# Kernel tuning notes

Hardware: AMD Instinct MI355X
Metric: run time of the kernel (lower is better)

Reference implementation:

```python
import jax, jax.numpy as jnp
import numpy as np

B = 4096       # batch
D = 256        # num_features
H = 512        # proposal_hidden_units
K = 10         # mixture_components
C = 64         # context_units
L = 4          # proposal_residual_blocks
S = 10         # num_importance_samples (call default)
HEAD = 3 * K + C
LOG2PI = float(np.log(2.0 * np.pi))


def setup_inputs() -> dict:
    key = jax.random.key(0)
    ks = jax.random.split(key, 10)
    x = jax.random.normal(ks[0], (B, D), jnp.float32)
    observed_mask = (jax.random.uniform(ks[1], (B, D)) < 0.5).astype(jnp.float32)
    s_in = 1.0 / np.sqrt(2 * D)
    s_h = 1.0 / np.sqrt(H)
    W_in = (jax.random.normal(ks[2], (2 * D, H), jnp.float32) * s_in)
    b_in = jnp.zeros((H,), jnp.float32)
    W1 = jax.random.normal(ks[3], (L, H, H), jnp.float32) * s_h
    b1 = jnp.zeros((L, H), jnp.float32)
    W2 = jax.random.normal(ks[4], (L, H, H), jnp.float32) * s_h
    b2 = jnp.zeros((L, H), jnp.float32)
    W_fin = jax.random.normal(ks[5], (H, D * HEAD), jnp.float32) * s_h
    b_fin = jnp.zeros((D * HEAD,), jnp.float32)
    return {
        "x": x, "observed_mask": observed_mask,
        "W_in": W_in, "b_in": b_in,
        "W1": W1, "b1": b1, "W2": W2, "b2": b2,
        "W_fin": W_fin, "b_fin": b_fin,
        "num_importance_samples": S,
    }


def _proposal_params(x_o, observed_mask, W_in, b_in, W1, b1, W2, b2, W_fin, b_fin):
    # Residual MLP proposal network on [x_o, observed_mask].
    h = jnp.concatenate([x_o, observed_mask], axis=-1) @ W_in + b_in  # [B, H]
    for l in range(L):
        r = jax.nn.relu(h) @ W1[l] + b1[l]
        r = jax.nn.relu(r) @ W2[l] + b2[l]
        h = h + r
    out = (h @ W_fin + b_fin).reshape(h.shape[0], D, HEAD)  # [B, D, 3K+C]
    logits = out[..., :K]
    means = out[..., K:2 * K]
    scales = jax.nn.softplus(out[..., 2 * K:3 * K]) + 1e-3
    return logits, means, scales


def reference(x, observed_mask, W_in, b_in, W1, b1, W2, b2, W_fin, b_fin,
              num_importance_samples):
    query = 1.0 - observed_mask
    x_o = x * observed_mask
    x_u = x * query

    logits, means, scales = _proposal_params(
        x_o, observed_mask, W_in, b_in, W1, b1, W2, b2, W_fin, b_fin)

    # Per-feature mixture-of-Gaussians log-likelihood of x_u, masked by query.
    log_w = jax.nn.log_softmax(logits, axis=-1)               # [B, D, K]
    z = (x_u[..., None] - means) / scales
    comp_ll = -0.5 * z * z - jnp.log(scales) - 0.5 * LOG2PI   # [B, D, K]
    proposal_ll = jax.scipy.special.logsumexp(log_w + comp_ll, axis=-1) * query

    # Samples (stop_gradient in the original).
    skey = jax.random.key(1234)
    kc, kn = jax.random.split(skey)
    comp = jax.random.categorical(kc, logits, axis=-1,
                                  shape=(num_importance_samples,) + logits.shape[:2])  # [S, B, D]
    mu = jnp.take_along_axis(means[None], comp[..., None], axis=-1)[..., 0]    # [S, B, D]
    sg = jnp.take_along_axis(scales[None], comp[..., None], axis=-1)[..., 0]   # [S, B, D]
    eps = jax.random.normal(kn, comp.shape, jnp.float32)
    samples = mu + sg * eps                                   # [S, B, D]
    samples = jnp.transpose(samples, (1, 0, 2))               # [B, S, D]
    samples = jax.lax.stop_gradient(samples) * query[:, None, :]
    # call() multiplies by query twice (before and after selected_features block)
    proposal_samples = samples * query[:, None, :]

    proposal_mean = jnp.sum(jax.nn.softmax(logits, axis=-1) * means, axis=-1) * query
    proposal_mean = proposal_mean * query  # second masking, as in call()

    return proposal_ll, proposal_samples, proposal_mean
```

## Files before the change

### kernel.cpp

```cpp
#include <hip/hip_runtime.h>
#include <cstdint>

#define B 4096
#define D 256
#define H 512
#define K 10
#define NL 4
#define S 10
#define NOUT 30
#define HEADW 94
#define ND (B*D)
#define NFIN 7680
#define NLOG 2560
#define NMS  5120

typedef __bf16 bf16x8 __attribute__((ext_vector_type(8)));
typedef float  f32x16 __attribute__((ext_vector_type(16)));

__host__ __device__ inline void threefry2x32(uint32_t k0, uint32_t k1,
                                             uint32_t x0, uint32_t x1,
                                             uint32_t& o0, uint32_t& o1) {
  uint32_t ks2 = k0 ^ k1 ^ 0x1BD11BDAu;
#define TF_ROT(x, r) (((x) << (r)) | ((x) >> (32 - (r))))
#define TF_RND(r) { x0 += x1; x1 = TF_ROT(x1, r); x1 ^= x0; }
  x0 += k0; x1 += k1;
  TF_RND(13) TF_RND(15) TF_RND(26) TF_RND(6)
  x0 += k1; x1 += ks2 + 1u;
  TF_RND(17) TF_RND(29) TF_RND(16) TF_RND(24)
  x0 += ks2; x1 += k0 + 2u;
  TF_RND(13) TF_RND(15) TF_RND(26) TF_RND(6)
  x0 += k0; x1 += k1 + 3u;
  TF_RND(17) TF_RND(29) TF_RND(16) TF_RND(24)
  x0 += k1; x1 += ks2 + 4u;
  TF_RND(13) TF_RND(15) TF_RND(26) TF_RND(6)
  x0 += ks2; x1 += k0 + 5u;
  o0 = x0; o1 = x1;
#undef TF_RND
#undef TF_ROT
}

__device__ __forceinline__ uint32_t rb32(uint32_t k0, uint32_t k1, uint32_t idx) {
  uint32_t a, b;
  threefry2x32(k0, k1, 0u, idx, a, b);
  return a ^ b;
}

__device__ __forceinline__ float u01_from_bits(uint32_t bits) {
  return __uint_as_float((bits >> 9) | 0x3f800000u) - 1.0f;
}

__device__ __forceinline__ float erfinv_f32(float x) {
  float w = -log1pf(-x * x);
  float p;
  if (w < 5.0f) {
    w = w - 2.5f;
    p = 2.81022636e-08f;
    p = fmaf(p, w, 3.43273939e-07f);
    p = fmaf(p, w, -3.5233877e-06f);
    p = fmaf(p, w, -4.39150654e-06f);
    p = fmaf(p, w, 0.00021858087f);
    p = fmaf(p, w, -0.00125372503f);
    p = fmaf(p, w, -0.00417768164f);
    p = fmaf(p, w, 0.246640727f);
    p = fmaf(p, w, 1.50140941f);
  } else {
    w = sqrtf(w) - 3.0f;
    p = -0.000200214257f;
    p = fmaf(p, w, 0.000100950558f);
    p = fmaf(p, w, 0.00134934322f);
    p = fmaf(p, w, -0.00367342844f);
    p = fmaf(p, w, 0.00573950773f);
    p = fmaf(p, w, -0.0076224613f);
    p = fmaf(p, w, 0.00943887047f);
    p = fmaf(p, w, 1.00167406f);
    p = fmaf(p, w, 2.83297682f);
  }
  return p * x;
}

__device__ __forceinline__ unsigned short bf16_rne(float x) {
  uint32_t u = __float_as_uint(x);
  uint32_t r = u + 0x7fffu + ((u >> 16) & 1u);
  return (unsigned short)(r >> 16);
}

__device__ __forceinline__ void split2(float x, short& hi, short& lo) {
  unsigned short hb = bf16_rne(x);
  float hf = __uint_as_float((uint32_t)hb << 16);
  hi = (short)hb;
  lo = (short)bf16_rne(x - hf);
}

__device__ __forceinline__ void gload16(const void* g, void* l) {
  __builtin_amdgcn_global_load_lds(
      (const __attribute__((address_space(1))) void*)g,
      (__attribute__((address_space(3))) void*)l, 16, 0, 0);
}

template <int ROWS>
__device__ __forceinline__ void stage_region(const short* __restrict__ g,
                                             short* l, int wid, int lane) {
#pragma unroll
  for (int c = wid; c < ROWS / 16; c += 4) {
    const short* gp = g + (size_t)(c * 16 + (lane >> 2)) * 512 + (lane & 3) * 8;
    gload16(gp, l + c * 512);
  }
}

__global__ __launch_bounds__(256) void prep_kernel(const float* __restrict__ x,
                                                   const float* __restrict__ mask,
                                                   float* __restrict__ xcat) {
  int i = blockIdx.x * 256 + threadIdx.x;
  if (i >= B * 2 * D) return;
  int b = i >> 9, c = i & 511;
  float v = (c < D) ? x[b * D + c] * mask[b * D + c] : mask[b * D + (c - D)];
  xcat[i] = v;
}

__global__ __launch_bounds__(256) void wgatherL(const float* __restrict__ Wf,
                                                float* __restrict__ wsgL) {
  int c = blockIdx.x * 256 + threadIdx.x;
  int k = blockIdx.y;
  int dd = c / K, j = c - dd * K;
  wsgL[(size_t)k * NLOG + c] = Wf[(size_t)k * (D * HEADW) + dd * HEADW + j];
}

__global__ __launch_bounds__(256) void wsplit_ms(const float* __restrict__ Wf,
                                                 short* __restrict__ whi,
                                                 short* __restrict__ wlo) {
  __shared__ float tile[32][33];
  int n0 = blockIdx.x * 32, k0 = blockIdx.y * 32;
  int tx = threadIdx.x & 31, ty = threadIdx.x >> 5;
#pragma unroll
  for (int r = 0; r < 4; ++r) {
    int k = k0 + ty + r * 8;
    int n = n0 + tx;
    int dd = n / 20, j = n - dd * 20;
    tile[ty + r * 8][tx] = Wf[(size_t)k * (D * HEADW) + dd * HEADW + 10 + j];
  }
  __syncthreads();
#pragma unroll
  for (int r = 0; r < 4; ++r) {
    int n = n0 + ty + r * 8;
    int k = k0 + tx;
    float v = tile[tx][ty + r * 8];
    short hb, lb;
    split2(v, hb, lb);
    whi[(size_t)n * 512 + k] = hb;
    wlo[(size_t)n * 512 + k] = lb;
  }
}

template <int RELU, int RES>
__global__ __launch_bounds__(256) void gemm_trunk(const float* __restrict__ A,
                                                  const float* __restrict__ W,
                                                  const float* __restrict__ bias,
                                                  const float* res, float* C) {
  __shared__ float As[64 * 68];
  __shared__ float Ws[64 * 64];
  const int tid = threadIdx.x;
  const int lane = tid & 63, wid = tid >> 6;
  const int tx = tid & 15, ty = tid >> 4;
  const int bm = blockIdx.y * 64, bn = blockIdx.x * 64;
  const int ls = tid & 15, lm = tid >> 4;

  float acc[4][4] = {};

  for (int k0 = 0; k0 < H; k0 += 64) {
#pragma unroll
    for (int c = wid; c < 16; c += 4) {
      gload16(W + (size_t)(k0 + c * 4 + (lane >> 4)) * H + bn + (lane & 15) * 4,
              Ws + c * 256 + lane * 4);
    }
#pragma unroll
    for (int r = 0; r < 4; ++r) {
      int m = lm + 16 * r;
      float4 f = *(const float4*)(A + (size_t)(bm + m) * H + k0 + 4 * ls);
      if (RELU) {
        f.x = fmaxf(f.x, 0.0f); f.y = fmaxf(f.y, 0.0f);
        f.z = fmaxf(f.z, 0.0f); f.w = fmaxf(f.w, 0.0f);
      }
      As[(4 * ls + 0) * 68 + m] = f.x;
      As[(4 * ls + 1) * 68 + m] = f.y;
      As[(4 * ls + 2) * 68 + m] = f.z;
      As[(4 * ls + 3) * 68 + m] = f.w;
    }
    __syncthreads();
#pragma unroll
    for (int kk = 0; kk < 64; ++kk) {
      float4 a4 = *(const float4*)(As + kk * 68 + ty * 4);
      float4 b4 = *(const float4*)(Ws + kk * 64 + tx * 4);
      float a[4] = {a4.x, a4.y, a4.z, a4.w};
      float b[4] = {b4.x, b4.y, b4.z, b4.w};
#pragma unroll
      for (int i = 0; i < 4; ++i)
#pragma unroll
        for (int j = 0; j < 4; ++j) acc[i][j] = fmaf(a[i], b[j], acc[i][j]);
    }
    __syncthreads();
  }
#pragma unroll
  for (int i = 0; i < 4; ++i) {
    int row = bm + ty * 4 + i;
#pragma unroll
    for (int j = 0; j < 4; ++j) {
      int col = bn + tx * 4 + j;
      float v = acc[i][j] + bias[col];
      if (RES) v = res[(size_t)row * H + col] + v;
      C[(size_t)row * H + col] = v;
    }
  }
}

__global__ __launch_bounds__(256) void gemm_head(const float* __restrict__ A,
                                                 const float* __restrict__ Wg,
                                                 const short* __restrict__ Bh,
                                                 const short* __restrict__ Bl,
                                                 const float* __restrict__ bf,
                                                 float* __restrict__ headout) {
  __shared__ __align__(16) float smem[8448];
  const int tid = threadIdx.x;
  const int lane = tid & 63, wid = tid >> 6;
  const int bm = blockIdx.y * 128;

  if (blockIdx.x < 20) {
    float* As = smem;
    float* Ws = smem + 4352;
    const int tx = tid & 15, ty = tid >> 4;
    const int bn = blockIdx.x * 128;
    const int ls = tid & 7, lm = tid >> 3;

    float acc[8][8] = {};

    for (int k0 = 0; k0 < H; k0 += 32) {
#pragma unroll
      for (int c = wid; c < 16; c += 4) {
        gload16(Wg + (size_t)(k0 + c * 2 + (lane >> 5)) * NLOG + bn + (lane & 31) * 4,
                Ws + c * 256 + lane * 4);
      }
#pragma unroll
      for (int r = 0; r < 4; ++r) {
        int m = lm + 32 * r;
        float4 f = *(const float4*)(A + (size_t)(bm + m) * H + k0 + 4 * ls);
        As[(4 * ls + 0) * 136 + m] = f.x;
        As[(4 * ls + 1) * 136 + m] = f.y;
        As[(4 * ls + 2) * 136 + m] = f.z;
        As[(4 * ls + 3) * 136 + m] = f.w;
      }
      __syncthreads();
#pragma unroll
      for (int kk = 0; kk < 32; ++kk) {
        float a[8], b[8];
        *(float4*)(a + 0) = *(const float4*)(As + kk * 136 + ty * 8);
        *(float4*)(a + 4) = *(const float4*)(As + kk * 136 + ty * 8 + 4);
        *(float4*)(b + 0) = *(const float4*)(Ws + kk * 128 + tx * 8);
        *(float4*)(b + 4) = *(const float4*)(Ws + kk * 128 + tx * 8 + 4);
#pragma unroll
        for (int i = 0; i < 8; ++i)
#pragma unroll
          for (int j = 0; j < 8; ++j) acc[i][j] = fmaf(a[i], b[j], acc[i][j]);
      }
      __syncthreads();
    }
#pragma unroll
    for (int i = 0; i < 8; ++i) {
      int row = bm + ty * 8 + i;
#pragma unroll
      for (int j = 0; j < 8; ++j) {
        int c = bn + tx * 8 + j;
        int dd = c / K, jj = c - dd * K;
        float v = acc[i][j] + bf[dd * HEADW + jj];
        headout[(size_t)row * NFIN + dd * NOUT + jj] = v;
      }
    }
  } else {
    short* lds = (short*)smem;
    const int wm = wid >> 1, wn = wid & 1;
    const int bn = (blockIdx.x - 20) * 128;
    const int ls = tid & 7, lm = tid >> 3;

    short* ldsAh = lds;
    short* ldsAl = lds + 4096;
    short* ldsBh = lds + 8192;
    short* ldsBl = lds + 12288;

    const short* gBh = Bh + (size_t)bn * 512;
    const short* gBl = Bl + (size_t)bn * 512;

    f32x16 acc[2][2];
#pragma unroll
    for (int mt = 0; mt < 2; ++mt)
#pragma unroll
      for (int nt = 0; nt < 2; ++nt)
#pragma unroll
        for (int i = 0; i < 16; ++i) acc[mt][nt][i] = 0.0f;

    for (int k0 = 0; k0 < 512; k0 += 32) {
      stage_region<128>(gBh + k0, ldsBh, wid, lane);
      stage_region<128>(gBl + k0, ldsBl, wid, lane);
#pragma unroll
      for (int r = 0; r < 4; ++r) {
        int m = lm + 32 * r;
        float4 f = *(const float4*)(A + (size_t)(bm + m) * H + k0 + 4 * ls);
        short4 h4, l4;
        split2(f.x, h4.x, l4.x); split2(f.y, h4.y, l4.y);
        split2(f.z, h4.z, l4.z); split2(f.w, h4.w, l4.w);
        *(short4*)(ldsAh + m * 32 + 4 * ls) = h4;
        *(short4*)(ldsAl + m * 32 + 4 * ls) = l4;
      }
      __syncthreads();
#pragma unroll
      for (int sub = 0; sub < 2; ++sub) {
        bf16x8 ah[2], al[2], bh[2], bl[2];
#pragma unroll
        for (int mt = 0; mt < 2; ++mt) {
          int r = wm * 64 + mt * 32 + (lane & 31);
          int off = r * 32 + sub * 16 + (lane >> 5) * 8;
          ah[mt] = *(const bf16x8*)(ldsAh + off);
          al[mt] = *(const bf16x8*)(ldsAl + off);
        }
#pragma unroll
        for (int nt = 0; nt < 2; ++nt) {
          int r = wn * 64 + nt * 32 + (lane & 31);
          int off = r * 32 + sub * 16 + (lane >> 5) * 8;
          bh[nt] = *(const bf16x8*)(ldsBh + off);
          bl[nt] = *(const bf16x8*)(ldsBl + off);
        }
#pragma unroll
        for (int mt = 0; mt < 2; ++mt)
#pragma unroll
          for (int nt = 0; nt < 2; ++nt) {
            acc[mt][nt] = __builtin_amdgcn_mfma_f32_32x32x16_bf16(ah[mt], bh[nt], acc[mt][nt], 0, 0, 0);
            acc[mt][nt] = __builtin_amdgcn_mfma_f32_32x32x16_bf16(ah[mt], bl[nt], acc[mt][nt], 0, 0, 0);
            acc[mt][nt] = __builtin_amdgcn_mfma_f32_32x32x16_bf16(al[mt], bh[nt], acc[mt][nt], 0, 0, 0);
          }
      }
      __syncthreads();
    }

#pragma unroll
    for (int mt = 0; mt < 2; ++mt)
#pragma unroll
      for (int nt = 0; nt < 2; ++nt) {
        int col = bn + wn * 64 + nt * 32 + (lane & 31);
        int rbase = bm + wm * 64 + mt * 32 + 4 * (lane >> 5);
        int dd = col / 20, j = col - dd * 20;
#pragma unroll
        for (int reg = 0; reg < 16; ++reg) {
          int row = rbase + (reg & 3) + 8 * (reg >> 2);
          float v = acc[mt][nt][reg] + bf[dd * HEADW + 10 + j];
          if (j >= 10) v = (fmaxf(v, 0.0f) + log1pf(expf(-fabsf(v)))) + 0.001f;
          headout[(size_t)row * NFIN + dd * NOUT + 10 + j] = v;
        }
      }
  }
}

__global__ __launch_bounds__(256) void init_counter(int* counter) {
  if (threadIdx.x == 0 && blockIdx.x == 0) *counter = 0;
}

__global__ __launch_bounds__(256) void compact_zero(const float* __restrict__ mask,
                                                    float* __restrict__ out_ll,
                                                    float* __restrict__ out_s,
                                                    float* __restrict__ out_mean,
                                                    int* __restrict__ list,
                                                    int* __restrict__ counter) {
  int idx = blockIdx.x * 256 + threadIdx.x;
  if (idx >= ND) return;
  if (mask[idx] != 0.0f) {
    int b = idx >> 8, d = idx & (D - 1);
    out_ll[idx] = 0.0f;
    out_mean[idx] = 0.0f;
#pragma unroll
    for (int s = 0; s < S; ++s) out_s[((size_t)b * S + s) * D + d] = 0.0f;
  } else {
    int pos = atomicAdd(counter, 1);
    list[pos] = idx;
  }
}

__global__ __launch_bounds__(256) void fused_tail(const float* __restrict__ head,
                                                  const float* __restrict__ x,
                                                  const float* __restrict__ mask,
                                                  const int* __restrict__ list,
                                                  const int* __restrict__ counter,
                                                  float* __restrict__ out_ll,
                                                  float* __restrict__ out_s,
                                                  float* __restrict__ out_mean,
                                                  uint32_t kc0, uint32_t kc1,
                                                  uint32_t kn0, uint32_t kn1) {
  int i = blockIdx.x * 256 + threadIdx.x;
  if (i >= *counter) return;
  int idx = list[i];
  int b = idx >> 8, d = idx & (D - 1);
  const float* hp = head + (size_t)idx * NOUT;
  float lg[K], mn[K], sc[K];
#pragma unroll
  for (int k = 0; k < K; ++k) { lg[k] = hp[k]; mn[k] = hp[K + k]; sc[k] = hp[2 * K + k]; }
  float q = 1.0f - mask[idx];
  float xu = x[idx] * q;
  float m = lg[0];
#pragma unroll
  for (int k = 1; k < K; ++k) m = fmaxf(m, lg[k]);
  float e[K];
  float sum = 0.0f;
#pragma unroll
  for (int k = 0; k < K; ++k) { e[k] = expf(lg[k] - m); sum += e[k]; }
  float lse = logf(sum);
  float a[K];
  float amax = -3.402823466e38f;
#pragma unroll
  for (int k = 0; k < K; ++k) {
    float z = (xu - mn[k]) / sc[k];
    float cll = -0.5f * z * z - logf(sc[k]) - 0.9189385332046727f;
    float lw = (lg[k] - m) - lse;
    a[k] = lw + cll;
    amax = fmaxf(amax, a[k]);
  }
  float s2 = 0.0f;
#pragma unroll
  for (int k = 0; k < K; ++k) s2 += expf(a[k] - amax);
  out_ll[idx] = (logf(s2) + amax) * q;
  float pm = 0.0f;
#pragma unroll
  for (int k = 0; k < K; ++k) pm += (e[k] / sum) * mn[k];
  out_mean[idx] = pm * q;
  float inv_e[K];
#pragma unroll
  for (int k = 0; k < K; ++k) inv_e[k] = 1.0f / e[k];
  for (int s = 0; s < S; ++s) {
    uint32_t t32 = (uint32_t)s * (uint32_t)ND + (uint32_t)idx;
    uint32_t base = t32 * (uint32_t)K;
    int best = 0;
    float rbest = 3.402823466e38f;
#pragma unroll
    for (int k = 0; k < K; ++k) {
      uint32_t bits = rb32(kc0, kc1, base + (uint32_t)k);
      float u = u01_from_bits(bits);
      float wv = -__log2f(u);
      float r = wv * inv_e[k];
      if (r < rbest) { rbest = r; best = k; }
    }
    uint32_t ebits = rb32(kn0, kn1, t32);
    float f = u01_from_bits(ebits);
    float r2 = f * 2.0f + (-0.99999994f);
    r2 = fmaxf(r2, -0.99999994f);
    float eps = 1.4142135623730951f * erfinv_f32(r2);
    out_s[((size_t)b * S + s) * D + d] = (mn[best] + sc[best] * eps) * q;
  }
}

extern "C" void kernel_launch(void* const* d_in, const int* in_sizes, int n_in,
                              void* d_out, int out_size, void* d_ws, size_t ws_size,
                              hipStream_t stream) {
  const float* x    = (const float*)d_in[0];
  const float* mask = (const float*)d_in[1];
  const float* W_in = (const float*)d_in[2];
  const float* b_in = (const float*)d_in[3];
  const float* W1   = (const float*)d_in[4];
  const float* b1   = (const float*)d_in[5];
  const float* W2   = (const float*)d_in[6];
  const float* b2   = (const float*)d_in[7];
  const float* Wf   = (const float*)d_in[8];
  const float* bf   = (const float*)d_in[9];

  char* w = (char*)d_ws;
  float* head   = (float*)w;
  float* xcat   = head;
  float* t      = head;
  float* h      = (float*)(w + 125829120);
  float* wsgL   = (float*)(w + 134217728);
  int*   list   = (int*)(w + 134217728);
  short* wms_h  = (short*)(w + 139460608);
  short* wms_l  = (short*)(w + 144703488);
  int*   counter = (int*)(w + 149946368);

  float* out_ll   = (float*)d_out;
  float* out_s    = out_ll + (size_t)ND;
  float* out_mean = out_s + (size_t)ND * S;

  wgatherL<<<dim3(NLOG / 256, 512), 256, 0, stream>>>(Wf, wsgL);
  wsplit_ms<<<dim3(NMS / 32, 512 / 32), 256, 0, stream>>>(Wf, wms_h, wms_l);

  prep_kernel<<<(B * 2 * D) / 256, 256, 0, stream>>>(x, mask, xcat);

  dim3 gtr(H / 64, B / 64);
  gemm_trunk<0, 0><<<gtr, 256, 0, stream>>>(xcat, W_in, b_in, nullptr, h);
  for (int l = 0; l < NL; ++l) {
    gemm_trunk<1, 0><<<gtr, 256, 0, stream>>>(h, W1 + (size_t)l * H * H,
                                              b1 + (size_t)l * H, nullptr, t);
    gemm_trunk<1, 1><<<gtr, 256, 0, stream>>>(t, W2 + (size_t)l * H * H,
                                              b2 + (size_t)l * H, h, h);
  }

  gemm_head<<<dim3(60, B / 128), 256, 0, stream>>>(h, wsgL, wms_h, wms_l, bf, head);

  init_counter<<<1, 256, 0, stream>>>(counter);
  compact_zero<<<ND / 256, 256, 0, stream>>>(mask, out_ll, out_s, out_mean,
                                             list, counter);

  uint32_t kc0, kc1, kn0, kn1;
  threefry2x32(0u, 1234u, 0u, 0u, kc0, kc1);
  threefry2x32(0u, 1234u, 0u, 1u, kn0, kn1);
  fused_tail<<<ND / 256, 256, 0, stream>>>(head, x, mask, list, counter,
                                           out_ll, out_s, out_mean,
                                           kc0, kc1, kn0, kn1);
}
```

Baseline: 1.213 ms.

## Pre-tile head weights for contiguous LDS staging and skip observed-feature stores

The split bf16 head weights are now stored pre-tiled in (n-block, k-chunk, sub, half, row, 8) order, so each k-step copies contiguous 512-short chunks into LDS. The A operand in LDS gets a matching layout, which changes the MFMA fragment reads and should reduce bank conflicts. The fp32 logits path reads B with a split tx*4 / 64+tx*4 pattern to avoid LDS conflicts. Both epilogues read the mask and skip writing head outputs for observed features, since the tail only uses query positions. This adds a mask load for every output element.

```diff
diff --git a/kernel.cpp b/kernel.cpp
--- a/kernel.cpp
+++ b/kernel.cpp
@@ -97,16 +97,6 @@
       (__attribute__((address_space(3))) void*)l, 16, 0, 0);
 }
 
-template <int ROWS>
-__device__ __forceinline__ void stage_region(const short* __restrict__ g,
-                                             short* l, int wid, int lane) {
-#pragma unroll
-  for (int c = wid; c < ROWS / 16; c += 4) {
-    const short* gp = g + (size_t)(c * 16 + (lane >> 2)) * 512 + (lane & 3) * 8;
-    gload16(gp, l + c * 512);
-  }
-}
-
 __global__ __launch_bounds__(256) void prep_kernel(const float* __restrict__ x,
                                                    const float* __restrict__ mask,
                                                    float* __restrict__ xcat) {
@@ -146,8 +136,11 @@
     float v = tile[tx][ty + r * 8];
     short hb, lb;
     split2(v, hb, lb);
-    whi[(size_t)n * 512 + k] = hb;
-    wlo[(size_t)n * 512 + k] = lb;
+    int nb = n >> 7, nl = n & 127;
+    int kc = k >> 5, sub = (k >> 4) & 1, kh = (k >> 3) & 1, e = k & 7;
+    size_t idx = ((((size_t)(nb * 16 + kc) * 4 + sub * 2 + kh) * 128 + nl) * 8) + e;
+    whi[idx] = hb;
+    wlo[idx] = lb;
   }
 }
 
@@ -217,6 +210,7 @@
                                                  const short* __restrict__ Bh,
                                                  const short* __restrict__ Bl,
                                                  const float* __restrict__ bf,
+                                                 const float* __restrict__ msk,
                                                  float* __restrict__ headout) {
   __shared__ __align__(16) float smem[8448];
   const int tid = threadIdx.x;
@@ -253,8 +247,8 @@
         float a[8], b[8];
         *(float4*)(a + 0) = *(const float4*)(As + kk * 136 + ty * 8);
         *(float4*)(a + 4) = *(const float4*)(As + kk * 136 + ty * 8 + 4);
-        *(float4*)(b + 0) = *(const float4*)(Ws + kk * 128 + tx * 8);
-        *(float4*)(b + 4) = *(const float4*)(Ws + kk * 128 + tx * 8 + 4);
+        *(float4*)(b + 0) = *(const float4*)(Ws + kk * 128 + tx * 4);
+        *(float4*)(b + 4) = *(const float4*)(Ws + kk * 128 + 64 + tx * 4);
 #pragma unroll
         for (int i = 0; i < 8; ++i)
 #pragma unroll
@@ -267,8 +261,9 @@
       int row = bm + ty * 8 + i;
 #pragma unroll
       for (int j = 0; j < 8; ++j) {
-        int c = bn + tx * 8 + j;
+        int c = bn + ((j < 4) ? (tx * 4 + j) : (64 + tx * 4 + (j - 4)));
         int dd = c / K, jj = c - dd * K;
+        if (msk[(size_t)row * D + dd] != 0.0f) continue;
         float v = acc[i][j] + bf[dd * HEADW + jj];
         headout[(size_t)row * NFIN + dd * NOUT + jj] = v;
       }
@@ -276,7 +271,7 @@
   } else {
     short* lds = (short*)smem;
     const int wm = wid >> 1, wn = wid & 1;
-    const int bn = (blockIdx.x - 20) * 128;
+    const int nb = blockIdx.x - 20;
     const int ls = tid & 7, lm = tid >> 3;
 
     short* ldsAh = lds;
@@ -284,8 +279,8 @@
     short* ldsBh = lds + 8192;
     short* ldsBl = lds + 12288;
 
-    const short* gBh = Bh + (size_t)bn * 512;
-    const short* gBl = Bl + (size_t)bn * 512;
+    const short* gBh = Bh + (size_t)nb * 65536;
+    const short* gBl = Bl + (size_t)nb * 65536;
 
     f32x16 acc[2][2];
 #pragma unroll
@@ -295,9 +290,15 @@
 #pragma unroll
         for (int i = 0; i < 16; ++i) acc[mt][nt][i] = 0.0f;
 
-    for (int k0 = 0; k0 < 512; k0 += 32) {
-      stage_region<128>(gBh + k0, ldsBh, wid, lane);
-      stage_region<128>(gBl + k0, ldsBl, wid, lane);
+    for (int kc = 0; kc < 16; ++kc) {
+      const short* cBh = gBh + kc * 4096;
+      const short* cBl = gBl + kc * 4096;
+#pragma unroll
+      for (int c = wid; c < 8; c += 4) {
+        gload16(cBh + c * 512 + lane * 8, ldsBh + c * 512);
+        gload16(cBl + c * 512 + lane * 8, ldsBl + c * 512);
+      }
+      int k0 = kc * 32;
 #pragma unroll
       for (int r = 0; r < 4; ++r) {
         int m = lm + 32 * r;
@@ -305,8 +306,9 @@
         short4 h4, l4;
         split2(f.x, h4.x, l4.x); split2(f.y, h4.y, l4.y);
         split2(f.z, h4.z, l4.z); split2(f.w, h4.w, l4.w);
-        *(short4*)(ldsAh + m * 32 + 4 * ls) = h4;
-        *(short4*)(ldsAl + m * 32 + 4 * ls) = l4;
+        int off = ((((ls >> 2) * 2 + ((ls >> 1) & 1)) * 128 + m) * 8) + (ls & 1) * 4;
+        *(short4*)(ldsAh + off) = h4;
+        *(short4*)(ldsAl + off) = l4;
       }
       __syncthreads();
 #pragma unroll
@@ -315,14 +317,14 @@
 #pragma unroll
         for (int mt = 0; mt < 2; ++mt) {
           int r = wm * 64 + mt * 32 + (lane & 31);
-          int off = r * 32 + sub * 16 + (lane >> 5) * 8;
+          int off = ((sub * 2 + (lane >> 5)) * 128 + r) * 8;
           ah[mt] = *(const bf16x8*)(ldsAh + off);
           al[mt] = *(const bf16x8*)(ldsAl + off);
         }
 #pragma unroll
         for (int nt = 0; nt < 2; ++nt) {
           int r = wn * 64 + nt * 32 + (lane & 31);
-          int off = r * 32 + sub * 16 + (lane >> 5) * 8;
+          int off = ((sub * 2 + (lane >> 5)) * 128 + r) * 8;
           bh[nt] = *(const bf16x8*)(ldsBh + off);
           bl[nt] = *(const bf16x8*)(ldsBl + off);
         }
@@ -342,12 +344,13 @@
     for (int mt = 0; mt < 2; ++mt)
 #pragma unroll
       for (int nt = 0; nt < 2; ++nt) {
-        int col = bn + wn * 64 + nt * 32 + (lane & 31);
+        int col = nb * 128 + wn * 64 + nt * 32 + (lane & 31);
         int rbase = bm + wm * 64 + mt * 32 + 4 * (lane >> 5);
         int dd = col / 20, j = col - dd * 20;
 #pragma unroll
         for (int reg = 0; reg < 16; ++reg) {
           int row = rbase + (reg & 3) + 8 * (reg >> 2);
+          if (msk[(size_t)row * D + dd] != 0.0f) continue;
           float v = acc[mt][nt][reg] + bf[dd * HEADW + 10 + j];
           if (j >= 10) v = (fmaxf(v, 0.0f) + log1pf(expf(-fabsf(v)))) + 0.001f;
           headout[(size_t)row * NFIN + dd * NOUT + 10 + j] = v;
@@ -494,7 +497,8 @@
                                               b2 + (size_t)l * H, h, h);
   }
 
-  gemm_head<<<dim3(60, B / 128), 256, 0, stream>>>(h, wsgL, wms_h, wms_l, bf, head);
+  gemm_head<<<dim3(60, B / 128), 256, 0, stream>>>(h, wsgL, wms_h, wms_l, bf,
+                                                   mask, head);
 
   init_counter<<<1, 256, 0, stream>>>(counter);
   compact_zero<<<ND / 256, 256, 0, stream>>>(mask, out_ll, out_s, out_mean,
```

New measurement: 1.314 ms. 8.4% more time.
